# Kernel tuning notes

Measured on AMD Instinct MI355X. Metric: run time of the kernel, lower is better.

## Reference

```python
import jax, jax.numpy as jnp
import numpy as np

HID = 512
ALPHA = 0.01
PI = np.float32(np.pi)


def _mlp(x, W0, b0, W1, b1, W2, b2, W3, b3):
    # x: [..., 2] -> scalar field u(x): [...]
    h = jnp.tanh(x @ W0 + b0)
    h = jnp.tanh(h @ W1 + b1)
    h = jnp.tanh(h @ W2 + b2)
    return (h @ W3 + b3)[..., 0]


def _forcing(x):
    # f = -Delta u for u = sin(pi x) sin(pi y^2)
    xx, yy = x[:, 0], x[:, 1]
    return (-PI ** 2 * (1 + 4 * yy ** 2) * jnp.sin(PI * xx) * jnp.sin(PI * yy ** 2)
            + 2 * PI * jnp.sin(PI * xx) * jnp.cos(PI * yy ** 2))


def setup_inputs() -> dict:
    key = jax.random.key(0)
    ks = jax.random.split(key, 6)
    n_i, n_b = 20000, 800
    x_interior = jax.random.uniform(ks[0], (n_i, 2), dtype=jnp.float32)  # domain (0,1)
    theta = jnp.linspace(0.0, 2.0 * np.pi, n_b)
    x_boundary = jnp.stack([(jnp.cos(theta) + 1.0) * 0.5,
                            (jnp.sin(theta) + 1.0) * 0.5], axis=1).astype(jnp.float32)

    def w(k, shape, fan_in):
        return (jax.random.normal(k, shape, jnp.float32) / np.float32(np.sqrt(fan_in)))

    W0 = w(ks[1], (2, HID), 2)
    b0 = jnp.zeros((HID,), jnp.float32)
    W1 = w(ks[2], (HID, HID), HID)
    b1 = jnp.zeros((HID,), jnp.float32)
    W2 = w(ks[3], (HID, HID), HID)
    b2 = jnp.zeros((HID,), jnp.float32)
    W3 = w(ks[4], (HID, 1), HID)
    b3 = jnp.zeros((1,), jnp.float32)
    return dict(x_interior=x_interior, x_boundary=x_boundary,
                W0=W0, b0=b0, W1=W1, b1=b1, W2=W2, b2=b2, W3=W3, b3=b3)


def reference(x_interior, x_boundary, W0, b0, W1, b1, W2, b2, W3, b3):
    params = (W0, b0, W1, b1, W2, b2, W3, b3)

    def u_scalar(x):  # x: [2] -> scalar
        return _mlp(x, *params)

    g = jax.grad(u_scalar)

    def lap_one(x):
        # Laplacian = trace of Hessian via forward-over-reverse HVPs
        lap = jnp.float32(0.0)
        for i in range(2):
            e = jnp.zeros((2,), x.dtype).at[i].set(1.0)
            _, hv = jax.jvp(g, (x,), (e,))
            lap = lap + hv[i]
        return lap

    laplacian = jax.vmap(lap_one)(x_interior)  # [n_interior]
    interior_loss = jnp.mean((laplacian - _forcing(x_interior)) ** 2)
    boundary_loss = jnp.mean(_mlp(x_boundary, *params) ** 2)
    total_loss = ALPHA * interior_loss + boundary_loss
    return total_loss, interior_loss, boundary_loss
```

## Files before the change

kernel.cpp:

```cpp
#include <hip/hip_runtime.h>
#include <math.h>

#define HID 512
#define PPB 32
#define SLAB 512

typedef __attribute__((ext_vector_type(8))) _Float16 half8;
typedef __attribute__((ext_vector_type(4))) _Float16 half4;
typedef __attribute__((ext_vector_type(4))) float f32x4;

static __device__ __forceinline__ float fast_tanh(float x) {
    float e = __expf(2.f * x);
    return 1.f - 2.f / (e + 1.f);
}


__global__ __launch_bounds__(256) void prep_wt(
    const float* __restrict__ W1, const float* __restrict__ W2,
    _Float16* __restrict__ W1h, _Float16* __restrict__ W2h)
{
    __shared__ float T[64][65];
    int b = blockIdx.x;
    const float* W = (b < 64) ? W1 : W2;
    _Float16* Wh   = (b < 64) ? W1h : W2h;
    int tb = b & 63;
    int jbG = tb >> 3, kbG = tb & 7;
    int j0 = jbG * 64, k0 = kbG * 64;
    int t = threadIdx.x;
    #pragma unroll
    for (int r = 0; r < 16; ++r) {
        int kl = r * 4 + (t >> 6);
        int jl = t & 63;
        T[kl][jl] = W[(size_t)(k0 + kl) * HID + j0 + jl];
    }
    __syncthreads();
    int ljb = t >> 6;
    int l15 = (t >> 2) & 15;
    int quad = t & 3;
    #pragma unroll
    for (int lkb = 0; lkb < 2; ++lkb) {
        half8 v;
        #pragma unroll
        for (int k8 = 0; k8 < 8; ++k8)
            v[k8] = (_Float16)T[lkb * 32 + quad * 8 + k8][ljb * 16 + l15];
        size_t out = (size_t)((jbG * 4 + ljb) * 16 + (kbG * 2 + lkb)) * SLAB
                   + (quad * 16 + l15) * 8;
        *(half8*)(Wh + out) = v;
    }
}

template<bool FULL>
static __device__ __forceinline__ void layer_pass(
    const _Float16* __restrict__ Wh, const float* __restrict__ bias,
    _Float16* Als, int wv, int lane)
{
    const int l15 = lane & 15, quad = lane >> 4;
    const int j0w = wv * 32;
    const int jb0 = wv * 2;
    const int loff = lane * 8;

    f32x4 acc[4][2][2];
    #pragma unroll
    for (int s = 0; s < 4; ++s)
        #pragma unroll
        for (int pf = 0; pf < 2; ++pf)
            #pragma unroll
            for (int jt = 0; jt < 2; ++jt) acc[s][pf][jt] = (f32x4)0.f;

    half8 wA[2], wB[2];
    #pragma unroll
    for (int jt = 0; jt < 2; ++jt)
        wA[jt] = *(const half8*)(Wh + (size_t)((jb0 + jt) * 16) * SLAB + loff);

    auto iter = [&](int kb, half8 (&wc)[2], half8 (&wn)[2]) {
        if (kb < 15) {
            #pragma unroll
            for (int jt = 0; jt < 2; ++jt)
                wn[jt] = *(const half8*)(Wh + (size_t)((jb0 + jt) * 16 + kb + 1) * SLAB + loff);
        }
        #pragma unroll
        for (int pf = 0; pf < 2; ++pf) {
            half8 a[4];
            #pragma unroll
            for (int s = 0; s < 4; ++s)
                a[s] = *(const half8*)(Als + ((s * 2 + pf) * 16 + kb) * SLAB + loff);
            #pragma unroll
            for (int s = 0; s < 4; ++s)
                #pragma unroll
                for (int jt = 0; jt < 2; ++jt)
                    acc[s][pf][jt] = __builtin_amdgcn_mfma_f32_16x16x32_f16(
                        wc[jt], a[s], acc[s][pf][jt], 0, 0, 0);
        }
    };

    #pragma unroll
    for (int kb = 0; kb < 16; kb += 2) {
        iter(kb,     wA, wB);
        iter(kb + 1, wB, wA);
    }

    __syncthreads();

    #pragma unroll
    for (int jt = 0; jt < 2; ++jt) {
        const int jbase = j0w + jt * 16 + quad * 4;
        const int qo = jt * 2 + (quad >> 1);
        const int e0 = (quad & 1) * 4;
        f32x4 bv = *(const f32x4*)&bias[jbase];
        #pragma unroll
        for (int pf = 0; pf < 2; ++pf) {
            half4 vh, vt1, vt2, vS;
            #pragma unroll
            for (int r = 0; r < 4; ++r) {
                float a  = fast_tanh(acc[0][pf][jt][r] + bv[r]);
                float g  = 1.f - a * a;
                float z1 = acc[1][pf][jt][r];
                float z2 = acc[2][pf][jt][r];
                vh[r] = (_Float16)a;
                if (FULL) {
                    vt1[r] = (_Float16)(g * z1);
                    vt2[r] = (_Float16)(g * z2);
                }
                vS[r] = (_Float16)(g * acc[3][pf][jt][r] - 2.f * a * g * (z1 * z1 + z2 * z2));
            }
            const int ooff = (qo * 16 + l15) * 8 + e0;
            *(half4*)(Als + ((0 * 2 + pf) * 16 + wv) * SLAB + ooff) = vh;
            if (FULL) {
                *(half4*)(Als + ((1 * 2 + pf) * 16 + wv) * SLAB + ooff) = vt1;
                *(half4*)(Als + ((2 * 2 + pf) * 16 + wv) * SLAB + ooff) = vt2;
            }
            *(half4*)(Als + ((3 * 2 + pf) * 16 + wv) * SLAB + ooff) = vS;
        }
    }
    __syncthreads();
}

__global__ __launch_bounds__(1024, 4) void pois_fused(
    const float* __restrict__ x_int, const float* __restrict__ x_bnd,
    const float* __restrict__ W0, const float* __restrict__ b0,
    const _Float16* __restrict__ W1h, const float* __restrict__ b1,
    const _Float16* __restrict__ W2h, const float* __restrict__ b2,
    const float* __restrict__ W3, const float* __restrict__ b3,
    float* __restrict__ partials, int NI, int NT, int nblk)
{
    __shared__ _Float16 Als[8 * 16 * SLAB];
    __shared__ float scU[16][32], scL[16][32], sc[64];

    const int tid = threadIdx.x;
    const int wv = tid >> 6, lane = tid & 63;
    const int l15 = lane & 15, quad = lane >> 4;
    const int p0 = blockIdx.x * PPB;

    #pragma unroll
    for (int ph = 0; ph < 2; ++ph) {
        const int p = ph * 16 + l15;
        int gp = p0 + p;
        int gpc = (gp >= NT) ? 0 : gp;
        float xx, yy;
        if (gpc < NI) { xx = x_int[2 * gpc];        yy = x_int[2 * gpc + 1]; }
        else          { xx = x_bnd[2 * (gpc - NI)]; yy = x_bnd[2 * (gpc - NI) + 1]; }
        const int k = wv * 32 + quad * 8;
        f32x4 w0a = *(const f32x4*)&W0[k],       w0b = *(const f32x4*)&W0[k + 4];
        f32x4 w1a = *(const f32x4*)&W0[HID + k], w1b = *(const f32x4*)&W0[HID + k + 4];
        f32x4 b0a = *(const f32x4*)&b0[k],       b0b = *(const f32x4*)&b0[k + 4];
        half8 vh, vt1, vt2, vS;
        #pragma unroll
        for (int e = 0; e < 8; ++e) {
            float w0i = (e < 4) ? w0a[e] : w0b[e - 4];
            float w1i = (e < 4) ? w1a[e] : w1b[e - 4];
            float bbi = (e < 4) ? b0a[e] : b0b[e - 4];
            float a = fast_tanh(xx * w0i + yy * w1i + bbi);
            float g = 1.f - a * a;
            vh[e]  = (_Float16)a;
            vt1[e] = (_Float16)(g * w0i);
            vt2[e] = (_Float16)(g * w1i);
            vS[e]  = (_Float16)(-2.f * a * g * (w0i * w0i + w1i * w1i));
        }
        const int off = lane * 8;
        *(half8*)(Als + ((0 * 2 + ph) * 16 + wv) * SLAB + off) = vh;
        *(half8*)(Als + ((1 * 2 + ph) * 16 + wv) * SLAB + off) = vt1;
        *(half8*)(Als + ((2 * 2 + ph) * 16 + wv) * SLAB + off) = vt2;
        *(half8*)(Als + ((3 * 2 + ph) * 16 + wv) * SLAB + off) = vS;
    }
    __syncthreads();

    layer_pass<true >(W1h, b1, Als, wv, lane);
    layer_pass<false>(W2h, b2, Als, wv, lane);

    {
        const int k = wv * 32 + quad * 8;
        f32x4 wa = *(const f32x4*)&W3[k], wb = *(const f32x4*)&W3[k + 4];
        #pragma unroll
        for (int ph = 0; ph < 2; ++ph) {
            half8 hh = *(const half8*)(Als + ((0 * 2 + ph) * 16 + wv) * SLAB + lane * 8);
            half8 ss = *(const half8*)(Als + ((3 * 2 + ph) * 16 + wv) * SLAB + lane * 8);
            float u = 0.f, lap = 0.f;
            #pragma unroll
            for (int e = 0; e < 4; ++e) {
                u   += (float)hh[e] * wa[e] + (float)hh[e + 4] * wb[e];
                lap += (float)ss[e] * wa[e] + (float)ss[e + 4] * wb[e];
            }
            u   += __shfl_xor(u, 16);   u   += __shfl_xor(u, 32);
            lap += __shfl_xor(lap, 16); lap += __shfl_xor(lap, 32);
            if (lane < 16) { scU[wv][ph * 16 + lane] = u; scL[wv][ph * 16 + lane] = lap; }
        }
    }
    __syncthreads();
    if (tid < 32) {
        const int p = tid;
        float u = 0.f, lap = 0.f;
        #pragma unroll
        for (int w = 0; w < 16; ++w) { u += scU[w][p]; lap += scL[w][p]; }
        int gp = p0 + p;
        float vi = 0.f, vb = 0.f;
        if (gp < NI) {
            const float PIf = 3.14159265358979323846f;
            float xx = x_int[2 * gp], yy = x_int[2 * gp + 1];
            float sx = sinf(PIf * xx);
            float y2 = yy * yy;
            float sy = sinf(PIf * y2), cy = cosf(PIf * y2);
            float f = -PIf * PIf * (1.f + 4.f * y2) * sx * sy + 2.f * PIf * sx * cy;
            float r = lap - f;
            vi = r * r;
        } else if (gp < NT) {
            float uu = u + b3[0];
            vb = uu * uu;
        }
        sc[p * 2] = vi; sc[p * 2 + 1] = vb;
    }
    __syncthreads();
    if (tid == 0) {
        float svi = 0.f, svb = 0.f;
        #pragma unroll
        for (int p = 0; p < PPB; ++p) { svi += sc[p * 2]; svb += sc[p * 2 + 1]; }
        partials[blockIdx.x] = svi;
        partials[nblk + blockIdx.x] = svb;
    }
}

__global__ __launch_bounds__(256) void pois_reduce(
    const float* __restrict__ partials, float* __restrict__ out,
    int nblk, int NI, int NB)
{
    int tid = threadIdx.x;
    float si = 0.f, sb = 0.f;
    for (int i = tid; i < nblk; i += 256) {
        si += partials[i];
        sb += partials[nblk + i];
    }
    #pragma unroll
    for (int off = 32; off > 0; off >>= 1) {
        si += __shfl_xor(si, off);
        sb += __shfl_xor(sb, off);
    }
    __shared__ float ri[4], rb[4];
    int wv = tid >> 6;
    if ((tid & 63) == 0) { ri[wv] = si; rb[wv] = sb; }
    __syncthreads();
    if (tid == 0) {
        float inter = (ri[0] + ri[1] + ri[2] + ri[3]) / (float)NI;
        float bound = (rb[0] + rb[1] + rb[2] + rb[3]) / (float)NB;
        out[0] = 0.01f * inter + bound;
        out[1] = inter;
        out[2] = bound;
    }
}

extern "C" void kernel_launch(void* const* d_in, const int* in_sizes, int n_in,
                              void* d_out, int out_size, void* d_ws, size_t ws_size,
                              hipStream_t stream)
{
    const float* x_int = (const float*)d_in[0];
    const float* x_bnd = (const float*)d_in[1];
    const float* W0 = (const float*)d_in[2];
    const float* b0 = (const float*)d_in[3];
    const float* W1 = (const float*)d_in[4];
    const float* b1 = (const float*)d_in[5];
    const float* W2 = (const float*)d_in[6];
    const float* b2 = (const float*)d_in[7];
    const float* W3 = (const float*)d_in[8];
    const float* b3 = (const float*)d_in[9];

    int NI = in_sizes[0] / 2;
    int NB = in_sizes[1] / 2;
    int NT = NI + NB;
    int nblk = (NT + PPB - 1) / PPB;

    float* partials = (float*)d_ws;
    _Float16* W1h = (_Float16*)((char*)d_ws + 16384);
    _Float16* W2h = W1h + 262144;

    prep_wt<<<128, 256, 0, stream>>>(W1, W2, W1h, W2h);

    pois_fused<<<nblk, 1024, 0, stream>>>(
        x_int, x_bnd, W0, b0, W1h, b1, W2h, b2, W3, b3,
        partials, NI, NT, nblk);

    pois_reduce<<<1, 256, 0, stream>>>(partials, (float*)d_out, nblk, NI, NB);
}
```

Measured before the change: 172.6 us.

## Software-pipeline layer phases across point halves and fold final reduction into fused kernel

Splits each hidden-layer pass into two per-half phases so that the tanh/derivative epilogue of one 16-point half is interleaved with the MFMA loop of the other half, hiding epilogue latency behind matrix work. Accumulators shrink to two per-half register sets that alternate roles. The separate reduction kernel is removed: the last block to finish, detected with an atomic counter (reset in the prep kernel) plus threadfences, performs the global sum. This adds register pressure and extra barriers, and depends on the counter reset ordering.

```diff
diff --git a/kernel.cpp b/kernel.cpp
--- a/kernel.cpp
+++ b/kernel.cpp
@@ -17,8 +17,10 @@
 
 __global__ __launch_bounds__(256) void prep_wt(
     const float* __restrict__ W1, const float* __restrict__ W2,
-    _Float16* __restrict__ W1h, _Float16* __restrict__ W2h)
-{
+    _Float16* __restrict__ W1h, _Float16* __restrict__ W2h,
+    unsigned* __restrict__ counter)
+{
+    if (blockIdx.x == 0 && threadIdx.x == 0) *counter = 0u;
     __shared__ float T[64][65];
     int b = blockIdx.x;
     const float* W = (b < 64) ? W1 : W2;
@@ -49,23 +51,52 @@
     }
 }
 
-template<bool FULL>
-static __device__ __forceinline__ void layer_pass(
-    const _Float16* __restrict__ Wh, const float* __restrict__ bias,
+template<int PHE, int MODE>
+static __device__ __forceinline__ void epi_one(
+    int jt, const f32x4 (&accE)[4][2], const float* __restrict__ biasE,
     _Float16* Als, int wv, int lane)
 {
     const int l15 = lane & 15, quad = lane >> 4;
-    const int j0w = wv * 32;
+    const int jbase = wv * 32 + jt * 16 + quad * 4;
+    const int qo = jt * 2 + (quad >> 1);
+    const int e0 = (quad & 1) * 4;
+    f32x4 bv = *(const f32x4*)&biasE[jbase];
+    half4 vh, vt1, vt2, vS;
+    #pragma unroll
+    for (int r = 0; r < 4; ++r) {
+        float a  = fast_tanh(accE[0][jt][r] + bv[r]);
+        float g  = 1.f - a * a;
+        float z1 = accE[1][jt][r];
+        float z2 = accE[2][jt][r];
+        vh[r] = (_Float16)a;
+        if constexpr (MODE == 1) {
+            vt1[r] = (_Float16)(g * z1);
+            vt2[r] = (_Float16)(g * z2);
+        }
+        vS[r] = (_Float16)(g * accE[3][jt][r] - 2.f * a * g * (z1 * z1 + z2 * z2));
+    }
+    const int ooff = (qo * 16 + l15) * 8 + e0;
+    *(half4*)(Als + ((0 * 2 + PHE) * 16 + wv) * SLAB + ooff) = vh;
+    if constexpr (MODE == 1) {
+        *(half4*)(Als + ((1 * 2 + PHE) * 16 + wv) * SLAB + ooff) = vt1;
+        *(half4*)(Als + ((2 * 2 + PHE) * 16 + wv) * SLAB + ooff) = vt2;
+    }
+    *(half4*)(Als + ((3 * 2 + PHE) * 16 + wv) * SLAB + ooff) = vS;
+}
+
+template<int PH, int PHE, int MODE>
+static __device__ __forceinline__ void layer_phase(
+    const _Float16* __restrict__ Wh, const float* __restrict__ biasE,
+    _Float16* Als, int wv, int lane,
+    f32x4 (&acc)[4][2], const f32x4 (&accE)[4][2])
+{
     const int jb0 = wv * 2;
     const int loff = lane * 8;
 
-    f32x4 acc[4][2][2];
     #pragma unroll
     for (int s = 0; s < 4; ++s)
         #pragma unroll
-        for (int pf = 0; pf < 2; ++pf)
-            #pragma unroll
-            for (int jt = 0; jt < 2; ++jt) acc[s][pf][jt] = (f32x4)0.f;
+        for (int jt = 0; jt < 2; ++jt) acc[s][jt] = (f32x4)0.f;
 
     half8 wA[2], wB[2];
     #pragma unroll
@@ -78,61 +109,93 @@
             for (int jt = 0; jt < 2; ++jt)
                 wn[jt] = *(const half8*)(Wh + (size_t)((jb0 + jt) * 16 + kb + 1) * SLAB + loff);
         }
-        #pragma unroll
-        for (int pf = 0; pf < 2; ++pf) {
-            half8 a[4];
+        half8 a[4];
+        #pragma unroll
+        for (int s = 0; s < 4; ++s)
+            a[s] = *(const half8*)(Als + ((s * 2 + PH) * 16 + kb) * SLAB + loff);
+        #pragma unroll
+        for (int s = 0; s < 4; ++s)
             #pragma unroll
-            for (int s = 0; s < 4; ++s)
-                a[s] = *(const half8*)(Als + ((s * 2 + pf) * 16 + kb) * SLAB + loff);
-            #pragma unroll
-            for (int s = 0; s < 4; ++s)
-                #pragma unroll
-                for (int jt = 0; jt < 2; ++jt)
-                    acc[s][pf][jt] = __builtin_amdgcn_mfma_f32_16x16x32_f16(
-                        wc[jt], a[s], acc[s][pf][jt], 0, 0, 0);
-        }
+            for (int jt = 0; jt < 2; ++jt)
+                acc[s][jt] = __builtin_amdgcn_mfma_f32_16x16x32_f16(
+                    wc[jt], a[s], acc[s][jt], 0, 0, 0);
     };
 
-    #pragma unroll
-    for (int kb = 0; kb < 16; kb += 2) {
-        iter(kb,     wA, wB);
-        iter(kb + 1, wB, wA);
-    }
-
-    __syncthreads();
-
-    #pragma unroll
-    for (int jt = 0; jt < 2; ++jt) {
-        const int jbase = j0w + jt * 16 + quad * 4;
-        const int qo = jt * 2 + (quad >> 1);
-        const int e0 = (quad & 1) * 4;
-        f32x4 bv = *(const f32x4*)&bias[jbase];
-        #pragma unroll
-        for (int pf = 0; pf < 2; ++pf) {
-            half4 vh, vt1, vt2, vS;
-            #pragma unroll
-            for (int r = 0; r < 4; ++r) {
-                float a  = fast_tanh(acc[0][pf][jt][r] + bv[r]);
-                float g  = 1.f - a * a;
-                float z1 = acc[1][pf][jt][r];
-                float z2 = acc[2][pf][jt][r];
-                vh[r] = (_Float16)a;
-                if (FULL) {
-                    vt1[r] = (_Float16)(g * z1);
-                    vt2[r] = (_Float16)(g * z2);
-                }
-                vS[r] = (_Float16)(g * acc[3][pf][jt][r] - 2.f * a * g * (z1 * z1 + z2 * z2));
-            }
-            const int ooff = (qo * 16 + l15) * 8 + e0;
-            *(half4*)(Als + ((0 * 2 + pf) * 16 + wv) * SLAB + ooff) = vh;
-            if (FULL) {
-                *(half4*)(Als + ((1 * 2 + pf) * 16 + wv) * SLAB + ooff) = vt1;
-                *(half4*)(Als + ((2 * 2 + pf) * 16 + wv) * SLAB + ooff) = vt2;
-            }
-            *(half4*)(Als + ((3 * 2 + pf) * 16 + wv) * SLAB + ooff) = vS;
-        }
-    }
-    __syncthreads();
+    iter(0, wA, wB);
+    iter(1, wB, wA);
+    iter(2, wA, wB);
+    if constexpr (MODE != 0) epi_one<PHE, MODE>(0, accE, biasE, Als, wv, lane);
+    iter(3, wB, wA);
+    iter(4, wA, wB);
+    iter(5, wB, wA);
+    iter(6, wA, wB);
+    iter(7, wB, wA);
+    iter(8, wA, wB);
+    if constexpr (MODE != 0) epi_one<PHE, MODE>(1, accE, biasE, Als, wv, lane);
+    iter(9, wB, wA);
+    iter(10, wA, wB);
+    iter(11, wB, wA);
+    iter(12, wA, wB);
+    iter(13, wB, wA);
+    iter(14, wA, wB);
+    iter(15, wB, wA);
+}
+
+static __device__ __forceinline__ void init_half(
+    int ph, const float* __restrict__ x_int, const float* __restrict__ x_bnd,
+    const float* __restrict__ W0, const float* __restrict__ b0,
+    _Float16* Als, int wv, int lane, int p0, int NI, int NT)
+{
+    const int l15 = lane & 15, quad = lane >> 4;
+    const int p = ph * 16 + l15;
+    int gp = p0 + p;
+    int gpc = (gp >= NT) ? 0 : gp;
+    float xx, yy;
+    if (gpc < NI) { xx = x_int[2 * gpc];        yy = x_int[2 * gpc + 1]; }
+    else          { xx = x_bnd[2 * (gpc - NI)]; yy = x_bnd[2 * (gpc - NI) + 1]; }
+    const int k = wv * 32 + quad * 8;
+    f32x4 w0a = *(const f32x4*)&W0[k],       w0b = *(const f32x4*)&W0[k + 4];
+    f32x4 w1a = *(const f32x4*)&W0[HID + k], w1b = *(const f32x4*)&W0[HID + k + 4];
+    f32x4 b0a = *(const f32x4*)&b0[k],       b0b = *(const f32x4*)&b0[k + 4];
+    half8 vh, vt1, vt2, vS;
+    #pragma unroll
+    for (int e = 0; e < 8; ++e) {
+        float w0i = (e < 4) ? w0a[e] : w0b[e - 4];
+        float w1i = (e < 4) ? w1a[e] : w1b[e - 4];
+        float bbi = (e < 4) ? b0a[e] : b0b[e - 4];
+        float a = fast_tanh(xx * w0i + yy * w1i + bbi);
+        float g = 1.f - a * a;
+        vh[e]  = (_Float16)a;
+        vt1[e] = (_Float16)(g * w0i);
+        vt2[e] = (_Float16)(g * w1i);
+        vS[e]  = (_Float16)(-2.f * a * g * (w0i * w0i + w1i * w1i));
+    }
+    const int off = lane * 8;
+    *(half8*)(Als + ((0 * 2 + ph) * 16 + wv) * SLAB + off) = vh;
+    *(half8*)(Als + ((1 * 2 + ph) * 16 + wv) * SLAB + off) = vt1;
+    *(half8*)(Als + ((2 * 2 + ph) * 16 + wv) * SLAB + off) = vt2;
+    *(half8*)(Als + ((3 * 2 + ph) * 16 + wv) * SLAB + off) = vS;
+}
+
+template<int PH>
+static __device__ __forceinline__ void final_half(
+    const float* __restrict__ W3, _Float16* Als, int wv, int lane,
+    float (*scU)[32], float (*scL)[32])
+{
+    const int quad = lane >> 4;
+    const int k = wv * 32 + quad * 8;
+    f32x4 wa = *(const f32x4*)&W3[k], wb = *(const f32x4*)&W3[k + 4];
+    half8 hh = *(const half8*)(Als + ((0 * 2 + PH) * 16 + wv) * SLAB + lane * 8);
+    half8 ss = *(const half8*)(Als + ((3 * 2 + PH) * 16 + wv) * SLAB + lane * 8);
+    float u = 0.f, lap = 0.f;
+    #pragma unroll
+    for (int e = 0; e < 4; ++e) {
+        u   += (float)hh[e] * wa[e] + (float)hh[e + 4] * wb[e];
+        lap += (float)ss[e] * wa[e] + (float)ss[e + 4] * wb[e];
+    }
+    u   += __shfl_xor(u, 16);   u   += __shfl_xor(u, 32);
+    lap += __shfl_xor(lap, 16); lap += __shfl_xor(lap, 32);
+    if (lane < 16) { scU[wv][PH * 16 + lane] = u; scL[wv][PH * 16 + lane] = lap; }
 }
 
 __global__ __launch_bounds__(1024, 4) void pois_fused(
@@ -141,71 +204,44 @@
     const _Float16* __restrict__ W1h, const float* __restrict__ b1,
     const _Float16* __restrict__ W2h, const float* __restrict__ b2,
     const float* __restrict__ W3, const float* __restrict__ b3,
-    float* __restrict__ partials, int NI, int NT, int nblk)
+    float* __restrict__ partials, unsigned* __restrict__ counter,
+    float* __restrict__ out, int NI, int NT, int nblk)
 {
     __shared__ _Float16 Als[8 * 16 * SLAB];
     __shared__ float scU[16][32], scL[16][32], sc[64];
+    __shared__ float ri[4], rb[4];
+    __shared__ int lastFlag;
 
     const int tid = threadIdx.x;
     const int wv = tid >> 6, lane = tid & 63;
-    const int l15 = lane & 15, quad = lane >> 4;
     const int p0 = blockIdx.x * PPB;
 
-    #pragma unroll
-    for (int ph = 0; ph < 2; ++ph) {
-        const int p = ph * 16 + l15;
-        int gp = p0 + p;
-        int gpc = (gp >= NT) ? 0 : gp;
-        float xx, yy;
-        if (gpc < NI) { xx = x_int[2 * gpc];        yy = x_int[2 * gpc + 1]; }
-        else          { xx = x_bnd[2 * (gpc - NI)]; yy = x_bnd[2 * (gpc - NI) + 1]; }
-        const int k = wv * 32 + quad * 8;
-        f32x4 w0a = *(const f32x4*)&W0[k],       w0b = *(const f32x4*)&W0[k + 4];
-        f32x4 w1a = *(const f32x4*)&W0[HID + k], w1b = *(const f32x4*)&W0[HID + k + 4];
-        f32x4 b0a = *(const f32x4*)&b0[k],       b0b = *(const f32x4*)&b0[k + 4];
-        half8 vh, vt1, vt2, vS;
-        #pragma unroll
-        for (int e = 0; e < 8; ++e) {
-            float w0i = (e < 4) ? w0a[e] : w0b[e - 4];
-            float w1i = (e < 4) ? w1a[e] : w1b[e - 4];
-            float bbi = (e < 4) ? b0a[e] : b0b[e - 4];
-            float a = fast_tanh(xx * w0i + yy * w1i + bbi);
-            float g = 1.f - a * a;
-            vh[e]  = (_Float16)a;
-            vt1[e] = (_Float16)(g * w0i);
-            vt2[e] = (_Float16)(g * w1i);
-            vS[e]  = (_Float16)(-2.f * a * g * (w0i * w0i + w1i * w1i));
-        }
-        const int off = lane * 8;
-        *(half8*)(Als + ((0 * 2 + ph) * 16 + wv) * SLAB + off) = vh;
-        *(half8*)(Als + ((1 * 2 + ph) * 16 + wv) * SLAB + off) = vt1;
-        *(half8*)(Als + ((2 * 2 + ph) * 16 + wv) * SLAB + off) = vt2;
-        *(half8*)(Als + ((3 * 2 + ph) * 16 + wv) * SLAB + off) = vS;
-    }
-    __syncthreads();
-
-    layer_pass<true >(W1h, b1, Als, wv, lane);
-    layer_pass<false>(W2h, b2, Als, wv, lane);
-
-    {
-        const int k = wv * 32 + quad * 8;
-        f32x4 wa = *(const f32x4*)&W3[k], wb = *(const f32x4*)&W3[k + 4];
-        #pragma unroll
-        for (int ph = 0; ph < 2; ++ph) {
-            half8 hh = *(const half8*)(Als + ((0 * 2 + ph) * 16 + wv) * SLAB + lane * 8);
-            half8 ss = *(const half8*)(Als + ((3 * 2 + ph) * 16 + wv) * SLAB + lane * 8);
-            float u = 0.f, lap = 0.f;
-            #pragma unroll
-            for (int e = 0; e < 4; ++e) {
-                u   += (float)hh[e] * wa[e] + (float)hh[e + 4] * wb[e];
-                lap += (float)ss[e] * wa[e] + (float)ss[e + 4] * wb[e];
-            }
-            u   += __shfl_xor(u, 16);   u   += __shfl_xor(u, 32);
-            lap += __shfl_xor(lap, 16); lap += __shfl_xor(lap, 32);
-            if (lane < 16) { scU[wv][ph * 16 + lane] = u; scL[wv][ph * 16 + lane] = lap; }
-        }
-    }
-    __syncthreads();
+    f32x4 accA[4][2], accB[4][2];
+
+    init_half(0, x_int, x_bnd, W0, b0, Als, wv, lane, p0, NI, NT);
+    __syncthreads();
+
+    layer_phase<0, 0, 0>(W1h, b1, Als, wv, lane, accA, accA);
+    init_half(1, x_int, x_bnd, W0, b0, Als, wv, lane, p0, NI, NT);
+    __syncthreads();
+
+    layer_phase<1, 0, 1>(W1h, b1, Als, wv, lane, accB, accA);
+    __syncthreads();
+
+    layer_phase<0, 1, 1>(W2h, b1, Als, wv, lane, accA, accB);
+    __syncthreads();
+
+    layer_phase<1, 0, 2>(W2h, b2, Als, wv, lane, accB, accA);
+    __syncthreads();
+
+    epi_one<1, 2>(0, accB, b2, Als, wv, lane);
+    epi_one<1, 2>(1, accB, b2, Als, wv, lane);
+    final_half<0>(W3, Als, wv, lane, scU, scL);
+    __syncthreads();
+
+    final_half<1>(W3, Als, wv, lane, scU, scL);
+    __syncthreads();
+
     if (tid < 32) {
         const int p = tid;
         float u = 0.f, lap = 0.f;
@@ -235,31 +271,33 @@
         for (int p = 0; p < PPB; ++p) { svi += sc[p * 2]; svb += sc[p * 2 + 1]; }
         partials[blockIdx.x] = svi;
         partials[nblk + blockIdx.x] = svb;
-    }
-}
-
-__global__ __launch_bounds__(256) void pois_reduce(
-    const float* __restrict__ partials, float* __restrict__ out,
-    int nblk, int NI, int NB)
-{
-    int tid = threadIdx.x;
-    float si = 0.f, sb = 0.f;
-    for (int i = tid; i < nblk; i += 256) {
-        si += partials[i];
-        sb += partials[nblk + i];
-    }
-    #pragma unroll
-    for (int off = 32; off > 0; off >>= 1) {
-        si += __shfl_xor(si, off);
-        sb += __shfl_xor(sb, off);
-    }
-    __shared__ float ri[4], rb[4];
-    int wv = tid >> 6;
-    if ((tid & 63) == 0) { ri[wv] = si; rb[wv] = sb; }
-    __syncthreads();
-    if (tid == 0) {
+        __threadfence();
+        unsigned old = atomicAdd(counter, 1u);
+        lastFlag = (old == (unsigned)(nblk - 1));
+    }
+    __syncthreads();
+
+    if (lastFlag) {
+        __threadfence();
+        if (tid < 256) {
+            float si = 0.f, sb = 0.f;
+            for (int i = tid; i < nblk; i += 256) {
+                si += partials[i];
+                sb += partials[nblk + i];
+            }
+            #pragma unroll
+            for (int off = 32; off > 0; off >>= 1) {
+                si += __shfl_xor(si, off);
+                sb += __shfl_xor(sb, off);
+            }
+            int w = tid >> 6;
+            if ((tid & 63) == 0) { ri[w] = si; rb[w] = sb; }
+        }
+    }
+    __syncthreads();
+    if (lastFlag && tid == 0) {
         float inter = (ri[0] + ri[1] + ri[2] + ri[3]) / (float)NI;
-        float bound = (rb[0] + rb[1] + rb[2] + rb[3]) / (float)NB;
+        float bound = (rb[0] + rb[1] + rb[2] + rb[3]) / (float)(NT - NI);
         out[0] = 0.01f * inter + bound;
         out[1] = inter;
         out[2] = bound;
@@ -285,16 +323,16 @@
     int NB = in_sizes[1] / 2;
     int NT = NI + NB;
     int nblk = (NT + PPB - 1) / PPB;
+    (void)NB;
 
     float* partials = (float*)d_ws;
+    unsigned* counter = (unsigned*)((char*)d_ws + 8192);
     _Float16* W1h = (_Float16*)((char*)d_ws + 16384);
     _Float16* W2h = W1h + 262144;
 
-    prep_wt<<<128, 256, 0, stream>>>(W1, W2, W1h, W2h);
+    prep_wt<<<128, 256, 0, stream>>>(W1, W2, W1h, W2h, counter);
 
     pois_fused<<<nblk, 1024, 0, stream>>>(
         x_int, x_bnd, W0, b0, W1h, b1, W2h, b2, W3, b3,
-        partials, NI, NT, nblk);
-
-    pois_reduce<<<1, 256, 0, stream>>>(partials, (float*)d_out, nblk, NI, NB);
-}
+        partials, counter, (float*)d_out, NI, NT, nblk);
+}
```

Result: slower. 208.1 us (+20.5%).

## Halve points per block, widen per-wave output tile, fuse final reduction via atomic counter

Applied to the files above, without the earlier changes.

Each block now handles 16 points with 512 threads instead of 32 with 1024. Each wave computes 64 output neurons (four 16-wide tiles) for all points, so every loaded weight fragment feeds more MFMAs and the shared activation buffer is half the size. The separate reduction kernel is removed: the last block to finish, found with an atomic counter reset in prep_wt, sums the partials and writes the loss. The cost is twice as many blocks, so W1/W2 are re-read from global/L2 more often overall, and the reduction now depends on a threadfence/atomic pattern.

```diff
diff --git a/kernel.cpp b/kernel.cpp
--- a/kernel.cpp
+++ b/kernel.cpp
@@ -2,7 +2,7 @@
 #include <math.h>
 
 #define HID 512
-#define PPB 32
+#define PPB 16
 #define SLAB 512
 
 typedef __attribute__((ext_vector_type(8))) _Float16 half8;
@@ -17,8 +17,10 @@
 
 __global__ __launch_bounds__(256) void prep_wt(
     const float* __restrict__ W1, const float* __restrict__ W2,
-    _Float16* __restrict__ W1h, _Float16* __restrict__ W2h)
+    _Float16* __restrict__ W1h, _Float16* __restrict__ W2h,
+    unsigned* __restrict__ counter)
 {
+    if (blockIdx.x == 0 && threadIdx.x == 0) *counter = 0u;
     __shared__ float T[64][65];
     int b = blockIdx.x;
     const float* W = (b < 64) ? W1 : W2;
@@ -55,42 +57,36 @@
     _Float16* Als, int wv, int lane)
 {
     const int l15 = lane & 15, quad = lane >> 4;
-    const int j0w = wv * 32;
-    const int jb0 = wv * 2;
+    const int jb0 = wv * 4;
     const int loff = lane * 8;
 
-    f32x4 acc[4][2][2];
+    f32x4 acc[4][4];
     #pragma unroll
     for (int s = 0; s < 4; ++s)
         #pragma unroll
-        for (int pf = 0; pf < 2; ++pf)
-            #pragma unroll
-            for (int jt = 0; jt < 2; ++jt) acc[s][pf][jt] = (f32x4)0.f;
-
-    half8 wA[2], wB[2];
-    #pragma unroll
-    for (int jt = 0; jt < 2; ++jt)
+        for (int jt = 0; jt < 4; ++jt) acc[s][jt] = (f32x4)0.f;
+
+    half8 wA[4], wB[4];
+    #pragma unroll
+    for (int jt = 0; jt < 4; ++jt)
         wA[jt] = *(const half8*)(Wh + (size_t)((jb0 + jt) * 16) * SLAB + loff);
 
-    auto iter = [&](int kb, half8 (&wc)[2], half8 (&wn)[2]) {
+    auto iter = [&](int kb, half8 (&wc)[4], half8 (&wn)[4]) {
         if (kb < 15) {
             #pragma unroll
-            for (int jt = 0; jt < 2; ++jt)
+            for (int jt = 0; jt < 4; ++jt)
                 wn[jt] = *(const half8*)(Wh + (size_t)((jb0 + jt) * 16 + kb + 1) * SLAB + loff);
         }
-        #pragma unroll
-        for (int pf = 0; pf < 2; ++pf) {
-            half8 a[4];
-            #pragma unroll
-            for (int s = 0; s < 4; ++s)
-                a[s] = *(const half8*)(Als + ((s * 2 + pf) * 16 + kb) * SLAB + loff);
-            #pragma unroll
-            for (int s = 0; s < 4; ++s)
-                #pragma unroll
-                for (int jt = 0; jt < 2; ++jt)
-                    acc[s][pf][jt] = __builtin_amdgcn_mfma_f32_16x16x32_f16(
-                        wc[jt], a[s], acc[s][pf][jt], 0, 0, 0);
-        }
+        half8 a[4];
+        #pragma unroll
+        for (int s = 0; s < 4; ++s)
+            a[s] = *(const half8*)(Als + (s * 16 + kb) * SLAB + loff);
+        #pragma unroll
+        for (int s = 0; s < 4; ++s)
+            #pragma unroll
+            for (int jt = 0; jt < 4; ++jt)
+                acc[s][jt] = __builtin_amdgcn_mfma_f32_16x16x32_f16(
+                    wc[jt], a[s], acc[s][jt], 0, 0, 0);
     };
 
     #pragma unroll
@@ -102,85 +98,88 @@
     __syncthreads();
 
     #pragma unroll
-    for (int jt = 0; jt < 2; ++jt) {
-        const int jbase = j0w + jt * 16 + quad * 4;
-        const int qo = jt * 2 + (quad >> 1);
+    for (int jt = 0; jt < 4; ++jt) {
+        const int jbase = wv * 64 + jt * 16 + quad * 4;
+        const int kbp = wv * 2 + (jt >> 1);
+        const int qo = (jt & 1) * 2 + (quad >> 1);
         const int e0 = (quad & 1) * 4;
         f32x4 bv = *(const f32x4*)&bias[jbase];
-        #pragma unroll
-        for (int pf = 0; pf < 2; ++pf) {
-            half4 vh, vt1, vt2, vS;
-            #pragma unroll
-            for (int r = 0; r < 4; ++r) {
-                float a  = fast_tanh(acc[0][pf][jt][r] + bv[r]);
-                float g  = 1.f - a * a;
-                float z1 = acc[1][pf][jt][r];
-                float z2 = acc[2][pf][jt][r];
-                vh[r] = (_Float16)a;
-                if (FULL) {
-                    vt1[r] = (_Float16)(g * z1);
-                    vt2[r] = (_Float16)(g * z2);
-                }
-                vS[r] = (_Float16)(g * acc[3][pf][jt][r] - 2.f * a * g * (z1 * z1 + z2 * z2));
-            }
-            const int ooff = (qo * 16 + l15) * 8 + e0;
-            *(half4*)(Als + ((0 * 2 + pf) * 16 + wv) * SLAB + ooff) = vh;
+        half4 vh, vt1, vt2, vS;
+        #pragma unroll
+        for (int r = 0; r < 4; ++r) {
+            float a  = fast_tanh(acc[0][jt][r] + bv[r]);
+            float g  = 1.f - a * a;
+            float z1 = acc[1][jt][r];
+            float z2 = acc[2][jt][r];
+            vh[r] = (_Float16)a;
             if (FULL) {
-                *(half4*)(Als + ((1 * 2 + pf) * 16 + wv) * SLAB + ooff) = vt1;
-                *(half4*)(Als + ((2 * 2 + pf) * 16 + wv) * SLAB + ooff) = vt2;
-            }
-            *(half4*)(Als + ((3 * 2 + pf) * 16 + wv) * SLAB + ooff) = vS;
-        }
-    }
-    __syncthreads();
-}
-
-__global__ __launch_bounds__(1024, 4) void pois_fused(
+                vt1[r] = (_Float16)(g * z1);
+                vt2[r] = (_Float16)(g * z2);
+            }
+            vS[r] = (_Float16)(g * acc[3][jt][r] - 2.f * a * g * (z1 * z1 + z2 * z2));
+        }
+        const int ooff = (qo * 16 + l15) * 8 + e0;
+        *(half4*)(Als + (0 * 16 + kbp) * SLAB + ooff) = vh;
+        if (FULL) {
+            *(half4*)(Als + (1 * 16 + kbp) * SLAB + ooff) = vt1;
+            *(half4*)(Als + (2 * 16 + kbp) * SLAB + ooff) = vt2;
+        }
+        *(half4*)(Als + (3 * 16 + kbp) * SLAB + ooff) = vS;
+    }
+    __syncthreads();
+}
+
+__global__ __launch_bounds__(512, 4) void pois_fused(
     const float* __restrict__ x_int, const float* __restrict__ x_bnd,
     const float* __restrict__ W0, const float* __restrict__ b0,
     const _Float16* __restrict__ W1h, const float* __restrict__ b1,
     const _Float16* __restrict__ W2h, const float* __restrict__ b2,
     const float* __restrict__ W3, const float* __restrict__ b3,
-    float* __restrict__ partials, int NI, int NT, int nblk)
+    float* __restrict__ partials, unsigned* __restrict__ counter,
+    float* __restrict__ out, int NI, int NT, int nblk)
 {
-    __shared__ _Float16 Als[8 * 16 * SLAB];
-    __shared__ float scU[16][32], scL[16][32], sc[64];
+    __shared__ _Float16 Als[4 * 16 * SLAB];
+    __shared__ float scU[8][16], scL[8][16], sc[32];
+    __shared__ float ri[4], rb[4];
+    __shared__ int lastFlag;
 
     const int tid = threadIdx.x;
     const int wv = tid >> 6, lane = tid & 63;
     const int l15 = lane & 15, quad = lane >> 4;
     const int p0 = blockIdx.x * PPB;
 
-    #pragma unroll
-    for (int ph = 0; ph < 2; ++ph) {
-        const int p = ph * 16 + l15;
-        int gp = p0 + p;
+    {
+        int gp = p0 + l15;
         int gpc = (gp >= NT) ? 0 : gp;
         float xx, yy;
         if (gpc < NI) { xx = x_int[2 * gpc];        yy = x_int[2 * gpc + 1]; }
         else          { xx = x_bnd[2 * (gpc - NI)]; yy = x_bnd[2 * (gpc - NI) + 1]; }
-        const int k = wv * 32 + quad * 8;
-        f32x4 w0a = *(const f32x4*)&W0[k],       w0b = *(const f32x4*)&W0[k + 4];
-        f32x4 w1a = *(const f32x4*)&W0[HID + k], w1b = *(const f32x4*)&W0[HID + k + 4];
-        f32x4 b0a = *(const f32x4*)&b0[k],       b0b = *(const f32x4*)&b0[k + 4];
-        half8 vh, vt1, vt2, vS;
-        #pragma unroll
-        for (int e = 0; e < 8; ++e) {
-            float w0i = (e < 4) ? w0a[e] : w0b[e - 4];
-            float w1i = (e < 4) ? w1a[e] : w1b[e - 4];
-            float bbi = (e < 4) ? b0a[e] : b0b[e - 4];
-            float a = fast_tanh(xx * w0i + yy * w1i + bbi);
-            float g = 1.f - a * a;
-            vh[e]  = (_Float16)a;
-            vt1[e] = (_Float16)(g * w0i);
-            vt2[e] = (_Float16)(g * w1i);
-            vS[e]  = (_Float16)(-2.f * a * g * (w0i * w0i + w1i * w1i));
-        }
-        const int off = lane * 8;
-        *(half8*)(Als + ((0 * 2 + ph) * 16 + wv) * SLAB + off) = vh;
-        *(half8*)(Als + ((1 * 2 + ph) * 16 + wv) * SLAB + off) = vt1;
-        *(half8*)(Als + ((2 * 2 + ph) * 16 + wv) * SLAB + off) = vt2;
-        *(half8*)(Als + ((3 * 2 + ph) * 16 + wv) * SLAB + off) = vS;
+        #pragma unroll
+        for (int t = 0; t < 2; ++t) {
+            const int kb = wv * 2 + t;
+            const int k = kb * 32 + quad * 8;
+            f32x4 w0a = *(const f32x4*)&W0[k],       w0b = *(const f32x4*)&W0[k + 4];
+            f32x4 w1a = *(const f32x4*)&W0[HID + k], w1b = *(const f32x4*)&W0[HID + k + 4];
+            f32x4 b0a = *(const f32x4*)&b0[k],       b0b = *(const f32x4*)&b0[k + 4];
+            half8 vh, vt1, vt2, vS;
+            #pragma unroll
+            for (int e = 0; e < 8; ++e) {
+                float w0i = (e < 4) ? w0a[e] : w0b[e - 4];
+                float w1i = (e < 4) ? w1a[e] : w1b[e - 4];
+                float bbi = (e < 4) ? b0a[e] : b0b[e - 4];
+                float a = fast_tanh(xx * w0i + yy * w1i + bbi);
+                float g = 1.f - a * a;
+                vh[e]  = (_Float16)a;
+                vt1[e] = (_Float16)(g * w0i);
+                vt2[e] = (_Float16)(g * w1i);
+                vS[e]  = (_Float16)(-2.f * a * g * (w0i * w0i + w1i * w1i));
+            }
+            const int off = lane * 8;
+            *(half8*)(Als + (0 * 16 + kb) * SLAB + off) = vh;
+            *(half8*)(Als + (1 * 16 + kb) * SLAB + off) = vt1;
+            *(half8*)(Als + (2 * 16 + kb) * SLAB + off) = vt2;
+            *(half8*)(Als + (3 * 16 + kb) * SLAB + off) = vS;
+        }
     }
     __syncthreads();
 
@@ -188,29 +187,31 @@
     layer_pass<false>(W2h, b2, Als, wv, lane);
 
     {
-        const int k = wv * 32 + quad * 8;
-        f32x4 wa = *(const f32x4*)&W3[k], wb = *(const f32x4*)&W3[k + 4];
-        #pragma unroll
-        for (int ph = 0; ph < 2; ++ph) {
-            half8 hh = *(const half8*)(Als + ((0 * 2 + ph) * 16 + wv) * SLAB + lane * 8);
-            half8 ss = *(const half8*)(Als + ((3 * 2 + ph) * 16 + wv) * SLAB + lane * 8);
-            float u = 0.f, lap = 0.f;
+        float u = 0.f, lap = 0.f;
+        #pragma unroll
+        for (int t = 0; t < 2; ++t) {
+            const int kb = wv * 2 + t;
+            const int k = kb * 32 + quad * 8;
+            f32x4 wa = *(const f32x4*)&W3[k], wb = *(const f32x4*)&W3[k + 4];
+            half8 hh = *(const half8*)(Als + (0 * 16 + kb) * SLAB + lane * 8);
+            half8 ss = *(const half8*)(Als + (3 * 16 + kb) * SLAB + lane * 8);
             #pragma unroll
             for (int e = 0; e < 4; ++e) {
                 u   += (float)hh[e] * wa[e] + (float)hh[e + 4] * wb[e];
                 lap += (float)ss[e] * wa[e] + (float)ss[e + 4] * wb[e];
             }
-            u   += __shfl_xor(u, 16);   u   += __shfl_xor(u, 32);
-            lap += __shfl_xor(lap, 16); lap += __shfl_xor(lap, 32);
-            if (lane < 16) { scU[wv][ph * 16 + lane] = u; scL[wv][ph * 16 + lane] = lap; }
-        }
-    }
-    __syncthreads();
-    if (tid < 32) {
+        }
+        u   += __shfl_xor(u, 16);   u   += __shfl_xor(u, 32);
+        lap += __shfl_xor(lap, 16); lap += __shfl_xor(lap, 32);
+        if (lane < 16) { scU[wv][l15] = u; scL[wv][l15] = lap; }
+    }
+    __syncthreads();
+
+    if (tid < 16) {
         const int p = tid;
         float u = 0.f, lap = 0.f;
         #pragma unroll
-        for (int w = 0; w < 16; ++w) { u += scU[w][p]; lap += scL[w][p]; }
+        for (int w = 0; w < 8; ++w) { u += scU[w][p]; lap += scL[w][p]; }
         int gp = p0 + p;
         float vi = 0.f, vb = 0.f;
         if (gp < NI) {
@@ -235,31 +236,33 @@
         for (int p = 0; p < PPB; ++p) { svi += sc[p * 2]; svb += sc[p * 2 + 1]; }
         partials[blockIdx.x] = svi;
         partials[nblk + blockIdx.x] = svb;
-    }
-}
-
-__global__ __launch_bounds__(256) void pois_reduce(
-    const float* __restrict__ partials, float* __restrict__ out,
-    int nblk, int NI, int NB)
-{
-    int tid = threadIdx.x;
-    float si = 0.f, sb = 0.f;
-    for (int i = tid; i < nblk; i += 256) {
-        si += partials[i];
-        sb += partials[nblk + i];
-    }
-    #pragma unroll
-    for (int off = 32; off > 0; off >>= 1) {
-        si += __shfl_xor(si, off);
-        sb += __shfl_xor(sb, off);
-    }
-    __shared__ float ri[4], rb[4];
-    int wv = tid >> 6;
-    if ((tid & 63) == 0) { ri[wv] = si; rb[wv] = sb; }
-    __syncthreads();
-    if (tid == 0) {
+        __threadfence();
+        unsigned old = atomicAdd(counter, 1u);
+        lastFlag = (old == (unsigned)(nblk - 1));
+    }
+    __syncthreads();
+
+    if (lastFlag) {
+        __threadfence();
+        if (tid < 256) {
+            float si = 0.f, sb = 0.f;
+            for (int i = tid; i < nblk; i += 256) {
+                si += partials[i];
+                sb += partials[nblk + i];
+            }
+            #pragma unroll
+            for (int off = 32; off > 0; off >>= 1) {
+                si += __shfl_xor(si, off);
+                sb += __shfl_xor(sb, off);
+            }
+            int w = tid >> 6;
+            if ((tid & 63) == 0) { ri[w] = si; rb[w] = sb; }
+        }
+    }
+    __syncthreads();
+    if (lastFlag && tid == 0) {
         float inter = (ri[0] + ri[1] + ri[2] + ri[3]) / (float)NI;
-        float bound = (rb[0] + rb[1] + rb[2] + rb[3]) / (float)NB;
+        float bound = (rb[0] + rb[1] + rb[2] + rb[3]) / (float)(NT - NI);
         out[0] = 0.01f * inter + bound;
         out[1] = inter;
         out[2] = bound;
@@ -285,16 +288,16 @@
     int NB = in_sizes[1] / 2;
     int NT = NI + NB;
     int nblk = (NT + PPB - 1) / PPB;
+    (void)NB;
 
     float* partials = (float*)d_ws;
+    unsigned* counter = (unsigned*)((char*)d_ws + 12288);
     _Float16* W1h = (_Float16*)((char*)d_ws + 16384);
     _Float16* W2h = W1h + 262144;
 
-    prep_wt<<<128, 256, 0, stream>>>(W1, W2, W1h, W2h);
-
-    pois_fused<<<nblk, 1024, 0, stream>>>(
+    prep_wt<<<128, 256, 0, stream>>>(W1, W2, W1h, W2h, counter);
+
+    pois_fused<<<nblk, 512, 0, stream>>>(
         x_int, x_bnd, W0, b0, W1h, b1, W2h, b2, W3, b3,
-        partials, NI, NT, nblk);
-
-    pois_reduce<<<1, 256, 0, stream>>>(partials, (float*)d_out, nblk, NI, NB);
-}
+        partials, counter, (float*)d_out, NI, NT, nblk);
+}
```

Result: slower. 207.4 us (+20.1%).

## Fuse final reduction via last-block atomic counter and prefetch LDS activations

Applied to the files above, without the earlier changes.

Removes the separate reduce kernel launch: each block bumps a global atomic counter after writing its partials, and the last block to arrive performs the final reduction and writes the outputs. The counter is zeroed in the weight-prep kernel. In the layer pass, activation fragments are now held in registers and the next k-slice is loaded from LDS right after each MFMA group, overlapping LDS reads with matrix math. This saves a kernel launch but adds register pressure and threadfence/atomic overhead in every block.

```diff
diff --git a/kernel.cpp b/kernel.cpp
--- a/kernel.cpp
+++ b/kernel.cpp
@@ -17,8 +17,10 @@
 
 __global__ __launch_bounds__(256) void prep_wt(
     const float* __restrict__ W1, const float* __restrict__ W2,
-    _Float16* __restrict__ W1h, _Float16* __restrict__ W2h)
+    _Float16* __restrict__ W1h, _Float16* __restrict__ W2h,
+    unsigned* __restrict__ counter)
 {
+    if (blockIdx.x == 0 && threadIdx.x == 0) *counter = 0u;
     __shared__ float T[64][65];
     int b = blockIdx.x;
     const float* W = (b < 64) ? W1 : W2;
@@ -55,7 +57,6 @@
     _Float16* Als, int wv, int lane)
 {
     const int l15 = lane & 15, quad = lane >> 4;
-    const int j0w = wv * 32;
     const int jb0 = wv * 2;
     const int loff = lane * 8;
 
@@ -72,6 +73,13 @@
     for (int jt = 0; jt < 2; ++jt)
         wA[jt] = *(const half8*)(Wh + (size_t)((jb0 + jt) * 16) * SLAB + loff);
 
+    half8 a[4][2];
+    #pragma unroll
+    for (int s = 0; s < 4; ++s)
+        #pragma unroll
+        for (int pf = 0; pf < 2; ++pf)
+            a[s][pf] = *(const half8*)(Als + ((s * 2 + pf) * 16 + 0) * SLAB + loff);
+
     auto iter = [&](int kb, half8 (&wc)[2], half8 (&wn)[2]) {
         if (kb < 15) {
             #pragma unroll
@@ -79,17 +87,16 @@
                 wn[jt] = *(const half8*)(Wh + (size_t)((jb0 + jt) * 16 + kb + 1) * SLAB + loff);
         }
         #pragma unroll
-        for (int pf = 0; pf < 2; ++pf) {
-            half8 a[4];
-            #pragma unroll
-            for (int s = 0; s < 4; ++s)
-                a[s] = *(const half8*)(Als + ((s * 2 + pf) * 16 + kb) * SLAB + loff);
-            #pragma unroll
-            for (int s = 0; s < 4; ++s)
+        for (int s = 0; s < 4; ++s) {
+            #pragma unroll
+            for (int pf = 0; pf < 2; ++pf) {
                 #pragma unroll
                 for (int jt = 0; jt < 2; ++jt)
                     acc[s][pf][jt] = __builtin_amdgcn_mfma_f32_16x16x32_f16(
-                        wc[jt], a[s], acc[s][pf][jt], 0, 0, 0);
+                        wc[jt], a[s][pf], acc[s][pf][jt], 0, 0, 0);
+                if (kb < 15)
+                    a[s][pf] = *(const half8*)(Als + ((s * 2 + pf) * 16 + kb + 1) * SLAB + loff);
+            }
         }
     };
 
@@ -103,7 +110,7 @@
 
     #pragma unroll
     for (int jt = 0; jt < 2; ++jt) {
-        const int jbase = j0w + jt * 16 + quad * 4;
+        const int jbase = wv * 32 + jt * 16 + quad * 4;
         const int qo = jt * 2 + (quad >> 1);
         const int e0 = (quad & 1) * 4;
         f32x4 bv = *(const f32x4*)&bias[jbase];
@@ -112,16 +119,16 @@
             half4 vh, vt1, vt2, vS;
             #pragma unroll
             for (int r = 0; r < 4; ++r) {
-                float a  = fast_tanh(acc[0][pf][jt][r] + bv[r]);
-                float g  = 1.f - a * a;
+                float a_ = fast_tanh(acc[0][pf][jt][r] + bv[r]);
+                float g  = 1.f - a_ * a_;
                 float z1 = acc[1][pf][jt][r];
                 float z2 = acc[2][pf][jt][r];
-                vh[r] = (_Float16)a;
+                vh[r] = (_Float16)a_;
                 if (FULL) {
                     vt1[r] = (_Float16)(g * z1);
                     vt2[r] = (_Float16)(g * z2);
                 }
-                vS[r] = (_Float16)(g * acc[3][pf][jt][r] - 2.f * a * g * (z1 * z1 + z2 * z2));
+                vS[r] = (_Float16)(g * acc[3][pf][jt][r] - 2.f * a_ * g * (z1 * z1 + z2 * z2));
             }
             const int ooff = (qo * 16 + l15) * 8 + e0;
             *(half4*)(Als + ((0 * 2 + pf) * 16 + wv) * SLAB + ooff) = vh;
@@ -141,10 +148,13 @@
     const _Float16* __restrict__ W1h, const float* __restrict__ b1,
     const _Float16* __restrict__ W2h, const float* __restrict__ b2,
     const float* __restrict__ W3, const float* __restrict__ b3,
-    float* __restrict__ partials, int NI, int NT, int nblk)
+    float* __restrict__ partials, unsigned* __restrict__ counter,
+    float* __restrict__ out, int NI, int NT, int nblk)
 {
     __shared__ _Float16 Als[8 * 16 * SLAB];
     __shared__ float scU[16][32], scL[16][32], sc[64];
+    __shared__ float ri[4], rb[4];
+    __shared__ int lastFlag;
 
     const int tid = threadIdx.x;
     const int wv = tid >> 6, lane = tid & 63;
@@ -206,6 +216,7 @@
         }
     }
     __syncthreads();
+
     if (tid < 32) {
         const int p = tid;
         float u = 0.f, lap = 0.f;
@@ -235,31 +246,33 @@
         for (int p = 0; p < PPB; ++p) { svi += sc[p * 2]; svb += sc[p * 2 + 1]; }
         partials[blockIdx.x] = svi;
         partials[nblk + blockIdx.x] = svb;
-    }
-}
-
-__global__ __launch_bounds__(256) void pois_reduce(
-    const float* __restrict__ partials, float* __restrict__ out,
-    int nblk, int NI, int NB)
-{
-    int tid = threadIdx.x;
-    float si = 0.f, sb = 0.f;
-    for (int i = tid; i < nblk; i += 256) {
-        si += partials[i];
-        sb += partials[nblk + i];
-    }
-    #pragma unroll
-    for (int off = 32; off > 0; off >>= 1) {
-        si += __shfl_xor(si, off);
-        sb += __shfl_xor(sb, off);
-    }
-    __shared__ float ri[4], rb[4];
-    int wv = tid >> 6;
-    if ((tid & 63) == 0) { ri[wv] = si; rb[wv] = sb; }
-    __syncthreads();
-    if (tid == 0) {
+        __threadfence();
+        unsigned old = atomicAdd(counter, 1u);
+        lastFlag = (old == (unsigned)(nblk - 1));
+    }
+    __syncthreads();
+
+    if (lastFlag) {
+        __threadfence();
+        if (tid < 256) {
+            float si = 0.f, sb = 0.f;
+            for (int i = tid; i < nblk; i += 256) {
+                si += partials[i];
+                sb += partials[nblk + i];
+            }
+            #pragma unroll
+            for (int off = 32; off > 0; off >>= 1) {
+                si += __shfl_xor(si, off);
+                sb += __shfl_xor(sb, off);
+            }
+            int w = tid >> 6;
+            if ((tid & 63) == 0) { ri[w] = si; rb[w] = sb; }
+        }
+    }
+    __syncthreads();
+    if (lastFlag && tid == 0) {
         float inter = (ri[0] + ri[1] + ri[2] + ri[3]) / (float)NI;
-        float bound = (rb[0] + rb[1] + rb[2] + rb[3]) / (float)NB;
+        float bound = (rb[0] + rb[1] + rb[2] + rb[3]) / (float)(NT - NI);
         out[0] = 0.01f * inter + bound;
         out[1] = inter;
         out[2] = bound;
@@ -285,16 +298,16 @@
     int NB = in_sizes[1] / 2;
     int NT = NI + NB;
     int nblk = (NT + PPB - 1) / PPB;
+    (void)NB;
 
     float* partials = (float*)d_ws;
+    unsigned* counter = (unsigned*)((char*)d_ws + 12288);
     _Float16* W1h = (_Float16*)((char*)d_ws + 16384);
     _Float16* W2h = W1h + 262144;
 
-    prep_wt<<<128, 256, 0, stream>>>(W1, W2, W1h, W2h);
+    prep_wt<<<128, 256, 0, stream>>>(W1, W2, W1h, W2h, counter);
 
     pois_fused<<<nblk, 1024, 0, stream>>>(
         x_int, x_bnd, W0, b0, W1h, b1, W2h, b2, W3, b3,
-        partials, NI, NT, nblk);
-
-    pois_reduce<<<1, 256, 0, stream>>>(partials, (float*)d_out, nblk, NI, NB);
-}
+        partials, counter, (float*)d_out, NI, NT, nblk);
+}
```

Result: slower. 256.9 us (+48.8%).
